# Optimization experiments

Measured on AMD Instinct MI355X. Metric: run time of the kernel, lower is better.

## Reference

```python
import jax, jax.numpy as jnp
import numpy as np

N_NODES = 100000


def gcn_conv(x, src, dst, deg_inv_sqrt, W, b, n):
    # GCNConv: h = D^{-1/2} (A + I) D^{-1/2} (x W) + b
    h = x @ W                                   # [N, out]
    norm = deg_inv_sqrt[src] * deg_inv_sqrt[dst]  # [E+N]
    msg = h[src] * norm[:, None]                # gather + scale
    out = jax.ops.segment_sum(msg, dst, num_segments=n)  # scatter-add
    return out + b


def setup_inputs() -> dict:
    key = jax.random.key(0)
    k1, k2, k3, k4 = jax.random.split(key, 4)
    N, E, IN, H, C = N_NODES, 1600000, 256, 128, 16
    x = jax.random.normal(k1, (N, IN), dtype=jnp.float32)
    edge_index = jax.random.randint(k2, (2, E), 0, N, dtype=jnp.int64)
    W1 = jax.random.normal(k3, (IN, H), dtype=jnp.float32) * (1.0 / np.sqrt(IN))
    b1 = jnp.zeros((H,), dtype=jnp.float32)
    W2 = jax.random.normal(k4, (H, C), dtype=jnp.float32) * (1.0 / np.sqrt(H))
    b2 = jnp.zeros((C,), dtype=jnp.float32)
    return {"x": x, "edge_index": edge_index, "W1": W1, "b1": b1, "W2": W2, "b2": b2}


def reference(x, edge_index, W1, b1, W2, b2):
    n = x.shape[0]
    loop = jnp.arange(n, dtype=edge_index.dtype)
    src = jnp.concatenate([edge_index[0], loop])  # add self-loops
    dst = jnp.concatenate([edge_index[1], loop])
    deg = jax.ops.segment_sum(jnp.ones_like(src, dtype=x.dtype), dst, num_segments=n)
    deg_inv_sqrt = jax.lax.rsqrt(deg)  # deg >= 1 due to self-loops

    h = gcn_conv(x, src, dst, deg_inv_sqrt, W1, b1, n)
    h = jax.nn.relu(h)
    # dropout is identity in eval mode
    out = gcn_conv(h, src, dst, deg_inv_sqrt, W2, b2, n)
    return jax.nn.log_softmax(out, axis=1)
```

## Files before the change

kernel.cpp:

```cpp
#include <hip/hip_runtime.h>
#include <math.h>

#define IN_DIM 256
#define H_DIM  128
#define C_DIM  16
#define BK_SHIFT 8
#define BK_CAP   6144
#define CHUNK    4096

typedef __attribute__((ext_vector_type(8))) short bf16x8;
typedef __attribute__((ext_vector_type(4))) float f32x4;

__device__ __forceinline__ ushort f2bf(float f) {
    uint u = __float_as_uint(f);
    u += 0x7fffu + ((u >> 16) & 1u);
    return (ushort)(u >> 16);
}
__device__ __forceinline__ float bflo(uint v) { return __uint_as_float(v << 16); }
__device__ __forceinline__ float bfhi(uint v) { return __uint_as_float(v & 0xffff0000u); }
__device__ __forceinline__ uint pk2(float a, float b) {
    return (uint)f2bf(a) | ((uint)f2bf(b) << 16);
}

__global__ __launch_bounds__(256) void k_prep(int* __restrict__ bcnt,
                                              const float* __restrict__ W1, ushort* __restrict__ W1T) {
    int b = blockIdx.x, t = threadIdx.x;
    if (b < 2) { bcnt[b * 256 + t] = 0; return; }
    int n = b - 2;
    W1T[n * 256 + t] = f2bf(W1[t * 128 + n]);
}

__global__ __launch_bounds__(256) void k_part(const int* __restrict__ esrc, const int* __restrict__ edst, int E,
                                              int* __restrict__ bcnt, int* __restrict__ part) {
    __shared__ int sh_cnt[512];
    __shared__ int sh_base[512];
    __shared__ int sh_gbase[512];
    __shared__ int sh_scan[256];
    __shared__ int2 sh_rec[CHUNK];
    int t = threadIdx.x;
    int c0 = blockIdx.x * CHUNK;
    int cnt = min(CHUNK, E - c0);
    sh_cnt[t] = 0; sh_cnt[t + 256] = 0;
    __syncthreads();
    int srcv[16], dstv[16], lrank[16];
#pragma unroll
    for (int j = 0; j < 16; j++) {
        int li = j * 256 + t;
        if (li < cnt) {
            srcv[j] = esrc[c0 + li]; dstv[j] = edst[c0 + li];
            lrank[j] = atomicAdd(&sh_cnt[dstv[j] >> BK_SHIFT], 1);
        }
    }
    __syncthreads();
    int pairsum = sh_cnt[2 * t] + sh_cnt[2 * t + 1];
    sh_scan[t] = pairsum;
    __syncthreads();
    for (int off = 1; off < 256; off <<= 1) {
        int x = 0;
        if (t >= off) x = sh_scan[t - off];
        __syncthreads();
        if (t >= off) sh_scan[t] += x;
        __syncthreads();
    }
    int excl = sh_scan[t] - pairsum;
    sh_base[2 * t] = excl;
    sh_base[2 * t + 1] = excl + sh_cnt[2 * t];
    __syncthreads();
    for (int b = t; b < 512; b += 256) {
        int c = sh_cnt[b];
        if (c > 0) sh_gbase[b] = atomicAdd(&bcnt[b], c);
    }
#pragma unroll
    for (int j = 0; j < 16; j++) {
        int li = j * 256 + t;
        if (li < cnt) {
            int b = dstv[j] >> BK_SHIFT;
            sh_rec[sh_base[b] + lrank[j]] = make_int2(srcv[j], dstv[j]);
        }
    }
    __syncthreads();
    for (int idx = t; idx < cnt; idx += 256) {
        int2 r = sh_rec[idx];
        int b = r.y >> BK_SHIFT;
        int pos = sh_gbase[b] + (idx - sh_base[b]);
        if (pos < BK_CAP)
            part[(size_t)b * BK_CAP + pos] = r.x | ((r.y & 255) << 20);
    }
}

__global__ __launch_bounds__(256) void k_bscan(const int* __restrict__ bcnt, int* __restrict__ bkbase,
                                               int* __restrict__ offsets, int N) {
    __shared__ int sh_scan[256];
    int t = threadIdx.x;
    int a0 = bcnt[2 * t], a1 = bcnt[2 * t + 1];
    int pairsum = a0 + a1;
    sh_scan[t] = pairsum;
    __syncthreads();
    for (int off = 1; off < 256; off <<= 1) {
        int x = 0;
        if (t >= off) x = sh_scan[t - off];
        __syncthreads();
        if (t >= off) sh_scan[t] += x;
        __syncthreads();
    }
    int excl = sh_scan[t] - pairsum;
    bkbase[2 * t] = excl;
    bkbase[2 * t + 1] = excl + a0;
    if (t == 255) offsets[N] = sh_scan[255];
}

__global__ __launch_bounds__(256) void k_bsort(const int* __restrict__ bcnt, const int* __restrict__ bkbase,
                                               const int* __restrict__ part,
                                               float* __restrict__ dis, int* __restrict__ offsets,
                                               int* __restrict__ csr, int N) {
    __shared__ int hist[256];
    __shared__ int run[256];
    __shared__ int srt[BK_CAP];
    int b = blockIdx.x, t = threadIdx.x;
    hist[t] = 0;
    __syncthreads();
    int cnt = min(bcnt[b], BK_CAP);
    const int* bp = &part[(size_t)b * BK_CAP];
    for (int idx = t; idx < cnt; idx += 256)
        atomicAdd(&hist[bp[idx] >> 20], 1);
    __syncthreads();
    int v = hist[t];
    run[t] = v;
    __syncthreads();
    for (int off = 1; off < 256; off <<= 1) {
        int x = 0;
        if (t >= off) x = run[t - off];
        __syncthreads();
        if (t >= off) run[t] += x;
        __syncthreads();
    }
    int start = run[t] - v;
    int base = bkbase[b];
    int node = b * 256 + t;
    if (node < N) {
        dis[node] = rsqrtf((float)(v + 1));
        offsets[node] = base + start;
    }
    __syncthreads();
    run[t] = start;
    __syncthreads();
    for (int idx = t; idx < cnt; idx += 256) {
        int r = bp[idx];
        int lpos = atomicAdd(&run[r >> 20], 1);
        srt[lpos] = r & 0xFFFFF;
    }
    __syncthreads();
    for (int idx = t; idx < cnt; idx += 256)
        csr[base + idx] = srt[idx];
}

__global__ __launch_bounds__(256) void k_gemm1(const float* __restrict__ x,
                                               const ushort* __restrict__ W1T,
                                               ushort* __restrict__ h1, int N) {
    __shared__ ushort Al[128 * 64];
    __shared__ ushort Bl[128 * 64];
    int tid = threadIdx.x;
    int lane = tid & 63, wid = tid >> 6;
    int wr = wid >> 1, wc = wid & 1;
    int r0 = blockIdx.x * 128;
    int row16 = lane & 15, kgrp = lane >> 4;

    f32x4 acc[4][4];
#pragma unroll
    for (int i = 0; i < 4; i++)
#pragma unroll
        for (int j = 0; j < 4; j++) acc[i][j] = (f32x4){0.f, 0.f, 0.f, 0.f};

    int srow = tid >> 1, shalf = tid & 1;

    for (int k0 = 0; k0 < 256; k0 += 64) {
        {
            int gr = r0 + srow;
            float4 f[8];
            if (gr < N) {
                const float* xp = &x[(size_t)gr * 256 + k0 + shalf * 32];
#pragma unroll
                for (int j = 0; j < 8; j++) f[j] = *(const float4*)&xp[j * 4];
            } else {
#pragma unroll
                for (int j = 0; j < 8; j++) f[j] = make_float4(0.f, 0.f, 0.f, 0.f);
            }
#pragma unroll
            for (int j = 0; j < 4; j++) {
                uint4 w;
                w.x = pk2(f[2 * j].x, f[2 * j].y);
                w.y = pk2(f[2 * j].z, f[2 * j].w);
                w.z = pk2(f[2 * j + 1].x, f[2 * j + 1].y);
                w.w = pk2(f[2 * j + 1].z, f[2 * j + 1].w);
                int idx = (srow * 64 + shalf * 32 + j * 8) ^ ((srow & 7) << 3);
                *(uint4*)&Al[idx] = w;
            }
        }
        {
            const ushort* wp = &W1T[srow * 256 + k0 + shalf * 32];
#pragma unroll
            for (int j = 0; j < 4; j++) {
                uint4 w = *(const uint4*)&wp[j * 8];
                int idx = (srow * 64 + shalf * 32 + j * 8) ^ ((srow & 7) << 3);
                *(uint4*)&Bl[idx] = w;
            }
        }
        __syncthreads();
#pragma unroll
        for (int kk = 0; kk < 2; kk++) {
            bf16x8 a[4], b[4];
#pragma unroll
            for (int mi = 0; mi < 4; mi++) {
                int r = wr * 64 + mi * 16 + row16;
                a[mi] = *(const bf16x8*)&Al[(r * 64 + kk * 32 + kgrp * 8) ^ ((r & 7) << 3)];
            }
#pragma unroll
            for (int ni = 0; ni < 4; ni++) {
                int c = wc * 64 + ni * 16 + row16;
                b[ni] = *(const bf16x8*)&Bl[(c * 64 + kk * 32 + kgrp * 8) ^ ((c & 7) << 3)];
            }
#pragma unroll
            for (int mi = 0; mi < 4; mi++)
#pragma unroll
                for (int ni = 0; ni < 4; ni++)
                    acc[mi][ni] = __builtin_amdgcn_mfma_f32_16x16x32_bf16(
                        a[mi], b[ni], acc[mi][ni], 0, 0, 0);
        }
        __syncthreads();
    }
#pragma unroll
    for (int mi = 0; mi < 4; mi++) {
        int rbase = r0 + wr * 64 + mi * 16 + kgrp * 4;
#pragma unroll
        for (int ni = 0; ni < 4; ni++) {
            int col = wc * 64 + ni * 16 + row16;
#pragma unroll
            for (int r = 0; r < 4; r++) {
                int gr = rbase + r;
                if (gr < N) h1[(size_t)gr * 128 + col] = f2bf(acc[mi][ni][r]);
            }
        }
    }
}

__global__ __launch_bounds__(256) void k_agg1(const ushort* __restrict__ h1,
                                              const float* __restrict__ dis,
                                              const int* __restrict__ off,
                                              const int* __restrict__ csr,
                                              const float* __restrict__ b1,
                                              const float* __restrict__ W2,
                                              ushort* __restrict__ h2, int N) {
    __shared__ float sh[4][128];
    int wave = threadIdx.x >> 6;
    int lane = threadIdx.x & 63;
    int node = blockIdx.x * 4 + wave;
    if (node >= N) return;

    int grp = lane >> 4, c = lane & 15;
    float w2r[32];
#pragma unroll
    for (int j = 0; j < 32; j++) w2r[j] = W2[(grp * 32 + j) * 16 + c];
    float2 bl = *(const float2*)&b1[lane * 2];

    float dd = dis[node];
    const uint* hp = (const uint*)h1;
    uint a = hp[(size_t)node * 64 + lane];
    float accx = bflo(a) * dd, accy = bfhi(a) * dd;

    int p0 = off[node], p1 = off[node + 1];
    for (int pb = p0; pb < p1; pb += 64) {
        int cnt = min(64, p1 - pb);
        int s = 0; float w = 0.f;
        if (lane < cnt) { s = csr[pb + lane]; w = dis[s]; }
        for (int j = 0; j < cnt; j += 16) {
            uint v[16]; float ww[16];
#pragma unroll
            for (int u = 0; u < 16; u++) {
                int idx = j + u;
                int ss = __shfl(s, idx);
                float t = __shfl(w, idx);
                bool pr = idx < cnt;
                ww[u] = pr ? t : 0.f;
                v[u] = pr ? hp[(size_t)ss * 64 + lane] : 0u;
            }
#pragma unroll
            for (int u = 0; u < 16; u++) {
                accx += bflo(v[u]) * ww[u];
                accy += bfhi(v[u]) * ww[u];
            }
        }
    }
    accx = fmaxf(accx * dd + bl.x, 0.f);
    accy = fmaxf(accy * dd + bl.y, 0.f);
    sh[wave][lane * 2]     = accx;
    sh[wave][lane * 2 + 1] = accy;
    float cs = 0.f;
#pragma unroll
    for (int j = 0; j < 32; j++) cs += sh[wave][grp * 32 + j] * w2r[j];
    cs += __shfl_xor(cs, 16);
    cs += __shfl_xor(cs, 32);
    if (lane < 16) h2[(size_t)node * 16 + lane] = f2bf(cs);
}

__global__ __launch_bounds__(256) void k_final(const ushort* __restrict__ h2,
                                               const float* __restrict__ b2,
                                               const float* __restrict__ dis,
                                               const int* __restrict__ off,
                                               const int* __restrict__ csr,
                                               float* __restrict__ out, int N) {
    int g = threadIdx.x >> 2;
    int q = threadIdx.x & 3;
    int node = blockIdx.x * 64 + g;
    if (node >= N) return;
    float dd = dis[node];
    uint2 v0 = *(const uint2*)&h2[(size_t)node * 16 + q * 4];
    float a0 = bflo(v0.x) * dd, a1 = bfhi(v0.x) * dd;
    float a2 = bflo(v0.y) * dd, a3 = bfhi(v0.y) * dd;
    int p0 = off[node], p1 = off[node + 1];
    for (int pb = p0; pb < p1; pb += 4) {
        int rem4 = p1 - pb;
        int cnt = rem4 < 4 ? rem4 : 4;
        int s = 0; float w = 0.f;
        if (q < cnt) { s = csr[pb + q]; w = dis[s]; }
        uint2 vv[4]; float ww[4];
#pragma unroll
        for (int u = 0; u < 4; u++) {
            int ss = __shfl(s, u, 4);
            float t = __shfl(w, u, 4);
            ww[u] = (u < cnt) ? t : 0.f;
            if (u < cnt) vv[u] = *(const uint2*)&h2[(size_t)ss * 16 + q * 4];
            else         vv[u] = make_uint2(0u, 0u);
        }
#pragma unroll
        for (int u = 0; u < 4; u++) {
            a0 += bflo(vv[u].x) * ww[u]; a1 += bfhi(vv[u].x) * ww[u];
            a2 += bflo(vv[u].y) * ww[u]; a3 += bfhi(vv[u].y) * ww[u];
        }
    }
    a0 = a0 * dd + b2[q * 4 + 0];
    a1 = a1 * dd + b2[q * 4 + 1];
    a2 = a2 * dd + b2[q * 4 + 2];
    a3 = a3 * dd + b2[q * 4 + 3];
    float m = fmaxf(fmaxf(a0, a1), fmaxf(a2, a3));
    m = fmaxf(m, __shfl_xor(m, 1, 4));
    m = fmaxf(m, __shfl_xor(m, 2, 4));
    float s4 = expf(a0 - m) + expf(a1 - m) + expf(a2 - m) + expf(a3 - m);
    s4 += __shfl_xor(s4, 1, 4);
    s4 += __shfl_xor(s4, 2, 4);
    float l = m + logf(s4);
    f32x4 o = {a0 - l, a1 - l, a2 - l, a3 - l};
    *(f32x4*)&out[(size_t)node * 16 + q * 4] = o;
}

extern "C" void kernel_launch(void* const* d_in, const int* in_sizes, int n_in,
                              void* d_out, int out_size, void* d_ws, size_t ws_size,
                              hipStream_t stream) {
    const float* x    = (const float*)d_in[0];
    const int*   eidx = (const int*)d_in[1];
    const float* W1   = (const float*)d_in[2];
    const float* b1   = (const float*)d_in[3];
    const float* W2   = (const float*)d_in[4];
    const float* b2   = (const float*)d_in[5];
    float* out = (float*)d_out;

    int N = in_sizes[0] / IN_DIM;
    int E = in_sizes[1] / 2;
    const int* esrc = eidx;
    const int* edst = eidx + E;

    char* ws = (char*)d_ws;
    size_t wo = 0;
    auto alloc = [&](size_t bytes) -> void* {
        void* p = ws + wo;
        wo = (wo + bytes + 255) & ~(size_t)255;
        return p;
    };
    int NB = (N + 255) >> 8;

    float*  dis     = (float*)alloc((size_t)N * 4);
    int*    offsets = (int*)alloc((size_t)(N + 1) * 4);
    int*    bcnt    = (int*)alloc(512 * 4);
    int*    bkbase  = (int*)alloc(512 * 4);
    int*    part    = (int*)alloc((size_t)NB * BK_CAP * 4);
    int*    csr     = (int*)alloc((size_t)E * 4);
    ushort* W1T     = (ushort*)alloc((size_t)IN_DIM * H_DIM * 2);
    ushort* h1      = (ushort*)alloc((size_t)N * H_DIM * 2);
    ushort* h2      = (ushort*)alloc((size_t)N * C_DIM * 2);

    k_prep  <<<130, 256, 0, stream>>>(bcnt, W1, W1T);
    k_part  <<<(E + CHUNK - 1) / CHUNK, 256, 0, stream>>>(esrc, edst, E, bcnt, part);
    k_bscan <<<1, 256, 0, stream>>>(bcnt, bkbase, offsets, N);
    k_bsort <<<NB, 256, 0, stream>>>(bcnt, bkbase, part, dis, offsets, csr, N);

    k_gemm1 <<<(N + 127) / 128, 256, 0, stream>>>(x, W1T, h1, N);
    k_agg1  <<<(N + 3) / 4, 256, 0, stream>>>(h1, dis, offsets, csr, b1, W2, h2, N);
    k_final <<<(N + 63) / 64, 256, 0, stream>>>(h2, b2, dis, offsets, csr, out, N);
}
```

Baseline: 199.6 us.

## Pre-scale features by source degree norm to drop per-edge weight gathers

After: 170.2 us. 14.8% less time.

```diff
diff --git a/kernel.cpp b/kernel.cpp
--- a/kernel.cpp
+++ b/kernel.cpp
@@ -156,6 +156,7 @@
 
 __global__ __launch_bounds__(256) void k_gemm1(const float* __restrict__ x,
                                                const ushort* __restrict__ W1T,
+                                               const float* __restrict__ dis,
                                                ushort* __restrict__ h1, int N) {
     __shared__ ushort Al[128 * 64];
     __shared__ ushort Bl[128 * 64];
@@ -231,13 +232,19 @@
 #pragma unroll
     for (int mi = 0; mi < 4; mi++) {
         int rbase = r0 + wr * 64 + mi * 16 + kgrp * 4;
+        float ds[4];
+#pragma unroll
+        for (int r = 0; r < 4; r++) {
+            int gr = rbase + r;
+            ds[r] = (gr < N) ? dis[gr] : 0.f;
+        }
 #pragma unroll
         for (int ni = 0; ni < 4; ni++) {
             int col = wc * 64 + ni * 16 + row16;
 #pragma unroll
             for (int r = 0; r < 4; r++) {
                 int gr = rbase + r;
-                if (gr < N) h1[(size_t)gr * 128 + col] = f2bf(acc[mi][ni][r]);
+                if (gr < N) h1[(size_t)gr * 128 + col] = f2bf(acc[mi][ni][r] * ds[r]);
             }
         }
     }
@@ -265,28 +272,39 @@
     float dd = dis[node];
     const uint* hp = (const uint*)h1;
     uint a = hp[(size_t)node * 64 + lane];
-    float accx = bflo(a) * dd, accy = bfhi(a) * dd;
+    float accx = bflo(a), accy = bfhi(a);
 
     int p0 = off[node], p1 = off[node + 1];
     for (int pb = p0; pb < p1; pb += 64) {
         int cnt = min(64, p1 - pb);
-        int s = 0; float w = 0.f;
-        if (lane < cnt) { s = csr[pb + lane]; w = dis[s]; }
-        for (int j = 0; j < cnt; j += 16) {
-            uint v[16]; float ww[16];
-#pragma unroll
-            for (int u = 0; u < 16; u++) {
-                int idx = j + u;
-                int ss = __shfl(s, idx);
-                float t = __shfl(w, idx);
-                bool pr = idx < cnt;
-                ww[u] = pr ? t : 0.f;
-                v[u] = pr ? hp[(size_t)ss * 64 + lane] : 0u;
-            }
-#pragma unroll
-            for (int u = 0; u < 16; u++) {
-                accx += bflo(v[u]) * ww[u];
-                accy += bfhi(v[u]) * ww[u];
+        int s = 0;
+        if (lane < cnt) s = csr[pb + lane];
+        int j = 0;
+        for (; j + 8 <= cnt; j += 8) {
+            uint v[8];
+#pragma unroll
+            for (int u = 0; u < 8; u++) {
+                int ss = __shfl(s, j + u);
+                v[u] = hp[(size_t)ss * 64 + lane];
+            }
+#pragma unroll
+            for (int u = 0; u < 8; u++) {
+                accx += bflo(v[u]);
+                accy += bfhi(v[u]);
+            }
+        }
+        int rem = cnt - j;
+        if (rem) {
+            uint v[8];
+#pragma unroll
+            for (int u = 0; u < 8; u++) {
+                int ss = __shfl(s, j + u);
+                v[u] = (u < rem) ? hp[(size_t)ss * 64 + lane] : 0u;
+            }
+#pragma unroll
+            for (int u = 0; u < 8; u++) {
+                accx += bflo(v[u]);
+                accy += bfhi(v[u]);
             }
         }
     }
@@ -299,7 +317,7 @@
     for (int j = 0; j < 32; j++) cs += sh[wave][grp * 32 + j] * w2r[j];
     cs += __shfl_xor(cs, 16);
     cs += __shfl_xor(cs, 32);
-    if (lane < 16) h2[(size_t)node * 16 + lane] = f2bf(cs);
+    if (lane < 16) h2[(size_t)node * 16 + lane] = f2bf(cs * dd);
 }
 
 __global__ __launch_bounds__(256) void k_final(const ushort* __restrict__ h2,
@@ -314,27 +332,25 @@
     if (node >= N) return;
     float dd = dis[node];
     uint2 v0 = *(const uint2*)&h2[(size_t)node * 16 + q * 4];
-    float a0 = bflo(v0.x) * dd, a1 = bfhi(v0.x) * dd;
-    float a2 = bflo(v0.y) * dd, a3 = bfhi(v0.y) * dd;
+    float a0 = bflo(v0.x), a1 = bfhi(v0.x);
+    float a2 = bflo(v0.y), a3 = bfhi(v0.y);
     int p0 = off[node], p1 = off[node + 1];
-    for (int pb = p0; pb < p1; pb += 4) {
-        int rem4 = p1 - pb;
-        int cnt = rem4 < 4 ? rem4 : 4;
-        int s = 0; float w = 0.f;
-        if (q < cnt) { s = csr[pb + q]; w = dis[s]; }
-        uint2 vv[4]; float ww[4];
-#pragma unroll
-        for (int u = 0; u < 4; u++) {
-            int ss = __shfl(s, u, 4);
-            float t = __shfl(w, u, 4);
-            ww[u] = (u < cnt) ? t : 0.f;
-            if (u < cnt) vv[u] = *(const uint2*)&h2[(size_t)ss * 16 + q * 4];
-            else         vv[u] = make_uint2(0u, 0u);
-        }
-#pragma unroll
-        for (int u = 0; u < 4; u++) {
-            a0 += bflo(vv[u].x) * ww[u]; a1 += bfhi(vv[u].x) * ww[u];
-            a2 += bflo(vv[u].y) * ww[u]; a3 += bfhi(vv[u].y) * ww[u];
+    for (int pb = p0; pb < p1; pb += 8) {
+        int cnt = min(8, p1 - pb);
+        int s0 = 0, s1 = 0;
+        if (q < cnt) s0 = csr[pb + q];
+        if (q + 4 < cnt) s1 = csr[pb + 4 + q];
+        uint2 vv[8];
+#pragma unroll
+        for (int u = 0; u < 8; u++) {
+            int ss = (u < 4) ? __shfl(s0, u, 4) : __shfl(s1, u - 4, 4);
+            vv[u] = (u < cnt) ? *(const uint2*)&h2[(size_t)ss * 16 + q * 4]
+                              : make_uint2(0u, 0u);
+        }
+#pragma unroll
+        for (int u = 0; u < 8; u++) {
+            a0 += bflo(vv[u].x); a1 += bfhi(vv[u].x);
+            a2 += bflo(vv[u].y); a3 += bfhi(vv[u].y);
         }
     }
     a0 = a0 * dd + b2[q * 4 + 0];
@@ -392,7 +408,7 @@
     k_bscan <<<1, 256, 0, stream>>>(bcnt, bkbase, offsets, N);
     k_bsort <<<NB, 256, 0, stream>>>(bcnt, bkbase, part, dis, offsets, csr, N);
 
-    k_gemm1 <<<(N + 127) / 128, 256, 0, stream>>>(x, W1T, h1, N);
+    k_gemm1 <<<(N + 127) / 128, 256, 0, stream>>>(x, W1T, dis, h1, N);
     k_agg1  <<<(N + 3) / 4, 256, 0, stream>>>(h1, dis, offsets, csr, b1, W2, h2, N);
     k_final <<<(N + 63) / 64, 256, 0, stream>>>(h2, b2, dis, offsets, csr, out, N);
 }
```
